# Kernel optimization log

Measured on AMD Instinct MI355X. Metric: run time of the kernel, lower is better.

The kernel has to match this reference:

```python
import jax, jax.numpy as jnp
import numpy as np
from jax import lax

B, T = 64, 2048
RNN, EMB, ATT, NF, K = 1024, 512, 128, 32, 31
PAD = (K - 1) // 2


def setup_inputs() -> dict:
    key = jax.random.key(0)
    ks = jax.random.split(key, 12)
    inp = {
        "attention_hidden_state": jax.random.normal(ks[0], (B, RNN), jnp.float32),
        "memory": jax.random.normal(ks[1], (B, T, EMB), jnp.float32),
        "processed_memory": jax.random.normal(ks[2], (B, T, ATT), jnp.float32),
        "attention_weights_cat": jax.random.uniform(ks[3], (B, 2, T), jnp.float32),
        "mask": jnp.zeros((B, T), dtype=bool),
        # query_layer: Linear(RNN -> ATT)
        "Wq": jax.random.normal(ks[4], (ATT, RNN), jnp.float32) / np.sqrt(RNN),
        "bq": jnp.zeros((ATT,), jnp.float32),
        # location conv: Conv1d(2 -> NF, kernel K, padding PAD)
        "conv_w": jax.random.normal(ks[5], (NF, 2, K), jnp.float32) / np.sqrt(2 * K),
        "conv_b": jnp.zeros((NF,), jnp.float32),
        # location dense: Linear(NF -> ATT)
        "Wl": jax.random.normal(ks[6], (ATT, NF), jnp.float32) / np.sqrt(NF),
        "bl": jnp.zeros((ATT,), jnp.float32),
        # v: Linear(ATT -> 1)
        "v_w": jax.random.normal(ks[7], (1, ATT), jnp.float32) / np.sqrt(ATT),
        "v_b": jnp.zeros((1,), jnp.float32),
    }
    return inp


def reference(attention_hidden_state, memory, processed_memory, attention_weights_cat,
              mask, Wq, bq, conv_w, conv_b, Wl, bl, v_w, v_b):
    # processed query: [B, 1, ATT]
    pq = (attention_hidden_state @ Wq.T + bq)[:, None, :]
    # location features: Conv1d over [B, 2, T] -> [B, NF, T]
    loc = lax.conv_general_dilated(
        attention_weights_cat, conv_w, window_strides=(1,),
        padding=[(PAD, PAD)], dimension_numbers=("NCH", "OIH", "NCH"))
    loc = loc + conv_b[None, :, None]
    # transpose to [B, T, NF], project to attention_dim: [B, T, ATT]
    loc = jnp.einsum("bft,af->bta", loc, Wl) + bl
    # energies: v(tanh(pq + loc + pm)) -> [B, T]
    energies = jnp.einsum("bta,a->bt", jnp.tanh(pq + loc + processed_memory), v_w[0]) + v_b[0]
    energies = jnp.where(mask, -jnp.inf, energies)
    attention_weights = jax.nn.softmax(energies, axis=1)  # [B, T]
    attention_context = jnp.einsum("bt,bte->be", attention_weights, memory)  # [B, EMB]
    return (attention_context, attention_weights)
```

## Files before the change

kernel.cpp:

```cpp
#include <hip/hip_runtime.h>
#include <math.h>

#define BB 64
#define TT 2048
#define RNN 1024
#define EMB 512
#define ATT 128
#define NF 32
#define KSZ 31
#define PAD 15

__global__ __launch_bounds__(256) void pq_kernel(
    const float* __restrict__ hidden, const float* __restrict__ Wq,
    const float* __restrict__ bq, const float* __restrict__ bl,
    float* __restrict__ pq)
{
    int b = blockIdx.x;
    __shared__ float h_s[RNN];
    int tid = threadIdx.x;
    for (int i = tid; i < RNN / 4; i += 256)
        reinterpret_cast<float4*>(h_s)[i] =
            reinterpret_cast<const float4*>(hidden + (size_t)b * RNN)[i];
    __syncthreads();
    int wave = tid >> 6, lane = tid & 63;
    int abase = blockIdx.y * 32;
    for (int a = abase + wave; a < abase + 32; a += 4) {
        const float4* wp = reinterpret_cast<const float4*>(Wq + (size_t)a * RNN);
        const float4* hp = reinterpret_cast<const float4*>(h_s);
        float acc = 0.f;
#pragma unroll
        for (int j = 0; j < 4; ++j) {
            float4 wv = wp[lane + 64 * j];
            float4 hv = hp[lane + 64 * j];
            acc += wv.x * hv.x + wv.y * hv.y + wv.z * hv.z + wv.w * hv.w;
        }
#pragma unroll
        for (int m = 32; m >= 1; m >>= 1) acc += __shfl_xor(acc, m);
        if (lane == 0) pq[b * ATT + a] = acc + bq[a] + bl[a];
    }
}

__device__ __forceinline__ float tanh_fast(float x) {
    float e2 = __expf(2.f * x);
    return 1.f - 2.f * __builtin_amdgcn_rcpf(e2 + 1.f);
}

template<int NH>
__global__ __launch_bounds__(256) void fused_kernel(
    const float* __restrict__ pm,
    const float* __restrict__ awc,
    const float* __restrict__ convw,
    const float* __restrict__ convb,
    const float* __restrict__ Wl,
    const float* __restrict__ vw,
    const float* __restrict__ vb,
    const float* __restrict__ pq,
    const float* __restrict__ memory,
    float* __restrict__ e_raw,
    float* __restrict__ part,
    float* __restrict__ ms)
{
    constexpr int TS = 64 * NH;
    const int TQv = TT / TS;
    int b  = blockIdx.x;
    int tq = blockIdx.y;
    int t0 = tq * TS;
    int tid = threadIdx.x;

    __shared__ float  awc_s[2][TS + KSZ - 1];
    __shared__ float  convw_s[NF * 2 * KSZ];
    __shared__ float  lf_s[TS][NF + 4];
    __shared__ float  e_s[64][65];
    __shared__ float  er_s[TS];
    __shared__ float  w_s[TS];
    __shared__ float  redm_s[16];
    __shared__ float4 red4_s[128];

    for (int i = tid; i < 2 * (TS + KSZ - 1); i += 256) {
        int c = i / (TS + KSZ - 1);
        int j = i - c * (TS + KSZ - 1);
        int t = t0 + j - PAD;
        awc_s[c][j] = (t >= 0 && t < TT) ? awc[((size_t)b * 2 + c) * TT + t] : 0.f;
    }
    for (int i = tid; i < NF * 2 * KSZ; i += 256)
        convw_s[i] = convw[i];
    __syncthreads();

    {
        int f = tid & 31;
        float w0[KSZ], w1[KSZ];
#pragma unroll
        for (int k = 0; k < KSZ; ++k) {
            w0[k] = convw_s[f * 2 * KSZ + k];
            w1[k] = convw_s[f * 2 * KSZ + KSZ + k];
        }
        float cb = convb[f];
#pragma unroll
        for (int half = 0; half < NH; ++half) {
            int tb = half * 64 + (tid >> 5) * 8;
            float out[8];
#pragma unroll
            for (int d = 0; d < 8; ++d) out[d] = cb;
#pragma unroll
            for (int j = 0; j < 8 + KSZ - 1; ++j) {
                float a0v = awc_s[0][tb + j];
                float a1v = awc_s[1][tb + j];
                int dlo = (j - (KSZ - 1) > 0) ? j - (KSZ - 1) : 0;
                int dhi = (j < 7) ? j : 7;
#pragma unroll
                for (int d = 0; d < 8; ++d)
                    if (d >= dlo && d <= dhi)
                        out[d] += w0[j - d] * a0v + w1[j - d] * a1v;
            }
#pragma unroll
            for (int d = 0; d < 8; ++d) lf_s[tb + d][f] = out[d];
        }
    }
    __syncthreads();

    int wave = tid >> 6, lane = tid & 63;
    int a0 = 2 * lane, a1 = a0 + 1;
    float4 wl0[NF / 4], wl1[NF / 4];
    {
        const float4* p0 = reinterpret_cast<const float4*>(Wl + (size_t)a0 * NF);
        const float4* p1 = reinterpret_cast<const float4*>(Wl + (size_t)a1 * NF);
#pragma unroll
        for (int j = 0; j < NF / 4; ++j) { wl0[j] = p0[j]; wl1[j] = p1[j]; }
    }
    float pq0 = pq[b * ATT + a0], pq1 = pq[b * ATT + a1];
    float v0  = vw[a0],           v1  = vw[a1];
    float vbv = vb[0];

#pragma unroll
    for (int half = 0; half < NH; ++half) {
        int tw = half * 64 + wave * 16;
        const float* pmb = pm + ((size_t)b * TT + t0 + tw) * ATT + a0;

        float2 pfA[8], pfB[8];
#pragma unroll
        for (int k = 0; k < 8; ++k)
            pfA[k] = *reinterpret_cast<const float2*>(pmb + (size_t)k * ATT);

#pragma unroll
        for (int i = 0; i < 8; ++i) {
            pfB[i] = *reinterpret_cast<const float2*>(pmb + (size_t)(8 + i) * ATT);
            int tl = tw + i;
            float lp0 = 0.f, lp1 = 0.f;
#pragma unroll
            for (int j = 0; j < NF / 4; ++j) {
                float4 lf = *reinterpret_cast<const float4*>(&lf_s[tl][4 * j]);
                lp0 += wl0[j].x * lf.x + wl0[j].y * lf.y + wl0[j].z * lf.z + wl0[j].w * lf.w;
                lp1 += wl1[j].x * lf.x + wl1[j].y * lf.y + wl1[j].z * lf.z + wl1[j].w * lf.w;
            }
            e_s[tl - half * 64][lane] = v0 * tanh_fast(pq0 + pfA[i].x + lp0)
                                      + v1 * tanh_fast(pq1 + pfA[i].y + lp1);
        }
#pragma unroll
        for (int i = 0; i < 8; ++i) {
            int tl = tw + 8 + i;
            float lp0 = 0.f, lp1 = 0.f;
#pragma unroll
            for (int j = 0; j < NF / 4; ++j) {
                float4 lf = *reinterpret_cast<const float4*>(&lf_s[tl][4 * j]);
                lp0 += wl0[j].x * lf.x + wl0[j].y * lf.y + wl0[j].z * lf.z + wl0[j].w * lf.w;
                lp1 += wl1[j].x * lf.x + wl1[j].y * lf.y + wl1[j].z * lf.z + wl1[j].w * lf.w;
            }
            e_s[tl - half * 64][lane] = v0 * tanh_fast(pq0 + pfB[i].x + lp0)
                                      + v1 * tanh_fast(pq1 + pfB[i].y + lp1);
        }
        __syncthreads();
        {
            int tl = tid >> 2, q = tid & 3;
            float s = 0.f;
#pragma unroll
            for (int k = 0; k < 16; ++k) s += e_s[tl][q * 16 + k];
            s += __shfl_xor(s, 1);
            s += __shfl_xor(s, 2);
            if (q == 0) {
                float raw = s + vbv;
                er_s[half * 64 + tl] = raw;
                e_raw[(size_t)b * TT + t0 + half * 64 + tl] = raw;
            }
        }
        __syncthreads();
    }

    {
        float v = (tid < TS) ? er_s[tid] : -INFINITY;
        float m = v;
#pragma unroll
        for (int d = 32; d >= 1; d >>= 1) m = fmaxf(m, __shfl_xor(m, d));
        if (NH == 2) {
            if ((tid & 63) == 0) redm_s[tid >> 6] = m;
            __syncthreads();
            m = fmaxf(redm_s[0], redm_s[1]);
        }
        float w = (tid < TS) ? __expf(v - m) : 0.f;
        if (tid < TS) w_s[tid] = w;
        float s = w;
#pragma unroll
        for (int d = 32; d >= 1; d >>= 1) s += __shfl_xor(s, d);
        if (NH == 2) {
            if ((tid & 63) == 0) redm_s[8 + (tid >> 6)] = s;
            __syncthreads();
            s = redm_s[8] + redm_s[9];
        }
        if (tid == 0) {
            ms[((size_t)b * TQv + tq) * 2 + 0] = m;
            ms[((size_t)b * TQv + tq) * 2 + 1] = s;
        }
    }
    __syncthreads();

    {
        int e4 = tid & 127, tr = tid >> 7;
        const float4* mp = reinterpret_cast<const float4*>(
            memory + ((size_t)(b * TT + t0 + tr)) * EMB) + e4;
        float4 acc = make_float4(0.f, 0.f, 0.f, 0.f);
#pragma unroll 8
        for (int i = 0; i < TS / 2; ++i) {
            float  w = w_s[2 * i + tr];
            float4 m = mp[(size_t)i * 2 * (EMB / 4)];
            acc.x += w * m.x; acc.y += w * m.y; acc.z += w * m.z; acc.w += w * m.w;
        }
        if (tr == 1) red4_s[e4] = acc;
        __syncthreads();
        if (tr == 0) {
            float4 o = red4_s[e4];
            acc.x += o.x; acc.y += o.y; acc.z += o.z; acc.w += o.w;
            reinterpret_cast<float4*>(part + ((size_t)tq * BB + b) * EMB)[e4] = acc;
        }
    }
}

template<int TQv>
__global__ __launch_bounds__(512) void finalize_kernel(
    const float* __restrict__ part, const float* __restrict__ ms,
    float* __restrict__ ctx, float* __restrict__ w_out)
{
    int b = blockIdx.x;
    int tid = threadIdx.x;
    __shared__ float scale_s[TQv];
    __shared__ float MS[2];
    if (tid < 64) {
        float m = (tid < TQv) ? ms[((size_t)b * TQv + tid) * 2 + 0] : -INFINITY;
        float s = (tid < TQv) ? ms[((size_t)b * TQv + tid) * 2 + 1] : 0.f;
        float M = m;
#pragma unroll
        for (int d = 32; d >= 1; d >>= 1) M = fmaxf(M, __shfl_xor(M, d));
        float sc = __expf(m - M);
        float Ssc = s * sc;
#pragma unroll
        for (int d = 32; d >= 1; d >>= 1) Ssc += __shfl_xor(Ssc, d);
        if (tid < TQv) scale_s[tid] = sc;
        if (tid == 0) { MS[0] = M; MS[1] = 1.f / Ssc; }
    }
    __syncthreads();
    float M = MS[0], invS = MS[1];
    {
        float acc = 0.f;
#pragma unroll
        for (int p = 0; p < TQv; ++p)
            acc += part[((size_t)p * BB + b) * EMB + tid] * scale_s[p];
        ctx[(size_t)b * EMB + tid] = acc * invS;
    }
#pragma unroll
    for (int k = 0; k < TT / 512; ++k) {
        size_t idx = (size_t)b * TT + k * 512 + tid;
        w_out[idx] = __expf(w_out[idx] - M) * invS;
    }
}

extern "C" void kernel_launch(void* const* d_in, const int* in_sizes, int n_in,
                              void* d_out, int out_size, void* d_ws, size_t ws_size,
                              hipStream_t stream)
{
    const float* hidden = (const float*)d_in[0];
    const float* memory = (const float*)d_in[1];
    const float* pm     = (const float*)d_in[2];
    const float* awc    = (const float*)d_in[3];
    const float* Wq     = (const float*)d_in[5];
    const float* bq     = (const float*)d_in[6];
    const float* convw  = (const float*)d_in[7];
    const float* convb  = (const float*)d_in[8];
    const float* Wl     = (const float*)d_in[9];
    const float* bl     = (const float*)d_in[10];
    const float* vw     = (const float*)d_in[11];
    const float* vb     = (const float*)d_in[12];

    float* out_ctx = (float*)d_out;
    float* out_w   = (float*)d_out + BB * EMB;

    float* ws = (float*)d_ws;
    float* pq = ws;

    pq_kernel<<<dim3(BB, 4), 256, 0, stream>>>(hidden, Wq, bq, bl, pq);

    size_t need32 = (size_t)(8192 + 32 * BB * EMB + BB * 32 * 2) * 4;
    if (ws_size >= need32) {
        const int TQ = 32;
        float* part  = ws + 8192;
        float* msbuf = part + (size_t)TQ * BB * EMB;
        fused_kernel<1><<<dim3(BB, TQ), 256, 0, stream>>>(
            pm, awc, convw, convb, Wl, vw, vb, pq, memory, out_w, part, msbuf);
        finalize_kernel<32><<<BB, 512, 0, stream>>>(part, msbuf, out_ctx, out_w);
    } else {
        const int TQ = 16;
        float* part  = ws + 8192;
        float* msbuf = part + (size_t)TQ * BB * EMB;
        fused_kernel<2><<<dim3(BB, TQ), 256, 0, stream>>>(
            pm, awc, convw, convb, Wl, vw, vb, pq, memory, out_w, part, msbuf);
        finalize_kernel<16><<<BB, 512, 0, stream>>>(part, msbuf, out_ctx, out_w);
    }
}
```

Before: 89.84 us.

## Warp-specialize fused attention kernel to overlap energy compute with context accumulation

Each block now covers 256 timesteps in four 64-row chunks. Waves 0-1 compute the energies for chunk h while waves 2-3 accumulate the weighted memory context for chunk h-1. An online softmax with running max and sum rescales the accumulator per chunk, and the grid shrinks to 8 time splits per batch, which cuts the partial buffers and finalize work. The cost is only half the waves doing each phase, fewer blocks (512), and serialized per-chunk barriers, which may underutilize the GPU.

```diff
diff --git a/kernel.cpp b/kernel.cpp
--- a/kernel.cpp
+++ b/kernel.cpp
@@ -9,6 +9,9 @@
 #define NF 32
 #define KSZ 31
 #define PAD 15
+#define TS 256
+#define HALVES 4
+#define TQV 8
 
 __global__ __launch_bounds__(256) void pq_kernel(
     const float* __restrict__ hidden, const float* __restrict__ Wq,
@@ -45,7 +48,6 @@
     return 1.f - 2.f * __builtin_amdgcn_rcpf(e2 + 1.f);
 }
 
-template<int NH>
 __global__ __launch_bounds__(256) void fused_kernel(
     const float* __restrict__ pm,
     const float* __restrict__ awc,
@@ -60,21 +62,18 @@
     float* __restrict__ part,
     float* __restrict__ ms)
 {
-    constexpr int TS = 64 * NH;
-    const int TQv = TT / TS;
     int b  = blockIdx.x;
     int tq = blockIdx.y;
     int t0 = tq * TS;
     int tid = threadIdx.x;
-
-    __shared__ float  awc_s[2][TS + KSZ - 1];
-    __shared__ float  convw_s[NF * 2 * KSZ];
-    __shared__ float  lf_s[TS][NF + 4];
-    __shared__ float  e_s[64][65];
-    __shared__ float  er_s[TS];
-    __shared__ float  w_s[TS];
-    __shared__ float  redm_s[16];
-    __shared__ float4 red4_s[128];
+    int wave = tid >> 6, lane = tid & 63;
+
+    __shared__ float awc_s[2][TS + KSZ - 1];
+    __shared__ float convw_s[NF * 2 * KSZ];
+    __shared__ float lf_s[TS][NF + 4];
+    __shared__ float e_s[64][68];
+    __shared__ float w_s[2][64];
+    __shared__ float sc_s[HALVES];
 
     for (int i = tid; i < 2 * (TS + KSZ - 1); i += 256) {
         int c = i / (TS + KSZ - 1);
@@ -95,8 +94,7 @@
             w1[k] = convw_s[f * 2 * KSZ + KSZ + k];
         }
         float cb = convb[f];
-#pragma unroll
-        for (int half = 0; half < NH; ++half) {
+        for (int half = 0; half < HALVES; ++half) {
             int tb = half * 64 + (tid >> 5) * 8;
             float out[8];
 #pragma unroll
@@ -116,135 +114,142 @@
             for (int d = 0; d < 8; ++d) lf_s[tb + d][f] = out[d];
         }
     }
-    __syncthreads();
-
-    int wave = tid >> 6, lane = tid & 63;
+
     int a0 = 2 * lane, a1 = a0 + 1;
     float4 wl0[NF / 4], wl1[NF / 4];
-    {
+    float pq0 = 0.f, pq1 = 0.f, v0 = 0.f, v1 = 0.f;
+    if (wave < 2) {
         const float4* p0 = reinterpret_cast<const float4*>(Wl + (size_t)a0 * NF);
         const float4* p1 = reinterpret_cast<const float4*>(Wl + (size_t)a1 * NF);
 #pragma unroll
         for (int j = 0; j < NF / 4; ++j) { wl0[j] = p0[j]; wl1[j] = p1[j]; }
-    }
-    float pq0 = pq[b * ATT + a0], pq1 = pq[b * ATT + a1];
-    float v0  = vw[a0],           v1  = vw[a1];
+        pq0 = pq[b * ATT + a0]; pq1 = pq[b * ATT + a1];
+        v0 = vw[a0]; v1 = vw[a1];
+    }
     float vbv = vb[0];
 
-#pragma unroll
-    for (int half = 0; half < NH; ++half) {
-        int tw = half * 64 + wave * 16;
-        const float* pmb = pm + ((size_t)b * TT + t0 + tw) * ATT + a0;
-
-        float2 pfA[8], pfB[8];
-#pragma unroll
-        for (int k = 0; k < 8; ++k)
-            pfA[k] = *reinterpret_cast<const float2*>(pmb + (size_t)k * ATT);
-
-#pragma unroll
-        for (int i = 0; i < 8; ++i) {
-            pfB[i] = *reinterpret_cast<const float2*>(pmb + (size_t)(8 + i) * ATT);
-            int tl = tw + i;
-            float lp0 = 0.f, lp1 = 0.f;
-#pragma unroll
-            for (int j = 0; j < NF / 4; ++j) {
-                float4 lf = *reinterpret_cast<const float4*>(&lf_s[tl][4 * j]);
-                lp0 += wl0[j].x * lf.x + wl0[j].y * lf.y + wl0[j].z * lf.z + wl0[j].w * lf.w;
-                lp1 += wl1[j].x * lf.x + wl1[j].y * lf.y + wl1[j].z * lf.z + wl1[j].w * lf.w;
-            }
-            e_s[tl - half * 64][lane] = v0 * tanh_fast(pq0 + pfA[i].x + lp0)
-                                      + v1 * tanh_fast(pq1 + pfA[i].y + lp1);
-        }
-#pragma unroll
-        for (int i = 0; i < 8; ++i) {
-            int tl = tw + 8 + i;
-            float lp0 = 0.f, lp1 = 0.f;
-#pragma unroll
-            for (int j = 0; j < NF / 4; ++j) {
-                float4 lf = *reinterpret_cast<const float4*>(&lf_s[tl][4 * j]);
-                lp0 += wl0[j].x * lf.x + wl0[j].y * lf.y + wl0[j].z * lf.z + wl0[j].w * lf.w;
-                lp1 += wl1[j].x * lf.x + wl1[j].y * lf.y + wl1[j].z * lf.z + wl1[j].w * lf.w;
-            }
-            e_s[tl - half * 64][lane] = v0 * tanh_fast(pq0 + pfB[i].x + lp0)
-                                      + v1 * tanh_fast(pq1 + pfB[i].y + lp1);
+    float m_run = -INFINITY, s_run = 0.f;
+    float4 acc = make_float4(0.f, 0.f, 0.f, 0.f);
+    int cidx = tid & 127;
+
+    __syncthreads();
+
+    for (int h = 0; h < HALVES; ++h) {
+        if (wave < 2) {
+            int rb = wave * 32;
+            const float* pmb = pm + ((size_t)b * TT + t0 + h * 64 + rb) * ATT + a0;
+            auto PROJ = [&](int r, float2 pmv) {
+                float lp0 = 0.f, lp1 = 0.f;
+#pragma unroll
+                for (int j = 0; j < NF / 4; ++j) {
+                    float4 lf = *reinterpret_cast<const float4*>(&lf_s[h * 64 + r][4 * j]);
+                    lp0 += wl0[j].x * lf.x + wl0[j].y * lf.y + wl0[j].z * lf.z + wl0[j].w * lf.w;
+                    lp1 += wl1[j].x * lf.x + wl1[j].y * lf.y + wl1[j].z * lf.z + wl1[j].w * lf.w;
+                }
+                e_s[r][lane] = v0 * tanh_fast(pq0 + pmv.x + lp0)
+                             + v1 * tanh_fast(pq1 + pmv.y + lp1);
+            };
+            float2 pfA[8], pfB[8];
+#pragma unroll
+            for (int k = 0; k < 8; ++k)
+                pfA[k] = *reinterpret_cast<const float2*>(pmb + (size_t)k * ATT);
+#pragma unroll
+            for (int i = 0; i < 8; ++i) {
+                pfB[i] = *reinterpret_cast<const float2*>(pmb + (size_t)(8 + i) * ATT);
+                PROJ(rb + i, pfA[i]);
+            }
+#pragma unroll
+            for (int i = 0; i < 8; ++i) {
+                pfA[i] = *reinterpret_cast<const float2*>(pmb + (size_t)(16 + i) * ATT);
+                PROJ(rb + 8 + i, pfB[i]);
+            }
+#pragma unroll
+            for (int i = 0; i < 8; ++i) {
+                pfB[i] = *reinterpret_cast<const float2*>(pmb + (size_t)(24 + i) * ATT);
+                PROJ(rb + 16 + i, pfA[i]);
+            }
+#pragma unroll
+            for (int i = 0; i < 8; ++i)
+                PROJ(rb + 24 + i, pfB[i]);
+        } else if (h >= 1) {
+            float sc = sc_s[h - 1];
+            acc.x *= sc; acc.y *= sc; acc.z *= sc; acc.w *= sc;
+            const float4* mp = reinterpret_cast<const float4*>(
+                memory + ((size_t)b * TT + t0 + (h - 1) * 64) * EMB) + cidx;
+#pragma unroll 8
+            for (int r = 0; r < 32; ++r) {
+                float w = w_s[(h - 1) & 1][r];
+                float4 m = mp[(size_t)r * (EMB / 4)];
+                acc.x += w * m.x; acc.y += w * m.y; acc.z += w * m.z; acc.w += w * m.w;
+            }
         }
         __syncthreads();
-        {
-            int tl = tid >> 2, q = tid & 3;
-            float s = 0.f;
-#pragma unroll
-            for (int k = 0; k < 16; ++k) s += e_s[tl][q * 16 + k];
-            s += __shfl_xor(s, 1);
-            s += __shfl_xor(s, 2);
-            if (q == 0) {
-                float raw = s + vbv;
-                er_s[half * 64 + tl] = raw;
-                e_raw[(size_t)b * TT + t0 + half * 64 + tl] = raw;
+
+        if (wave == 0) {
+            float4 s4 = make_float4(0.f, 0.f, 0.f, 0.f);
+#pragma unroll
+            for (int k = 0; k < 16; ++k) {
+                float4 x = *reinterpret_cast<const float4*>(&e_s[lane][4 * k]);
+                s4.x += x.x; s4.y += x.y; s4.z += x.z; s4.w += x.w;
+            }
+            float e = s4.x + s4.y + s4.z + s4.w + vbv;
+            e_raw[(size_t)b * TT + t0 + h * 64 + lane] = e;
+            float cm = e;
+#pragma unroll
+            for (int d = 32; d >= 1; d >>= 1) cm = fmaxf(cm, __shfl_xor(cm, d));
+            float m_new = fmaxf(m_run, cm);
+            float sc = __expf(m_run - m_new);
+            float wv = __expf(e - m_new);
+            w_s[h & 1][lane] = wv;
+            float ssum = wv;
+#pragma unroll
+            for (int d = 32; d >= 1; d >>= 1) ssum += __shfl_xor(ssum, d);
+            s_run = s_run * sc + ssum;
+            m_run = m_new;
+            if (lane == 0) sc_s[h] = sc;
+        } else if (wave >= 2 && h >= 1) {
+            const float4* mp = reinterpret_cast<const float4*>(
+                memory + ((size_t)b * TT + t0 + (h - 1) * 64) * EMB) + cidx;
+#pragma unroll 8
+            for (int r = 32; r < 64; ++r) {
+                float w = w_s[(h - 1) & 1][r];
+                float4 m = mp[(size_t)r * (EMB / 4)];
+                acc.x += w * m.x; acc.y += w * m.y; acc.z += w * m.z; acc.w += w * m.w;
             }
         }
         __syncthreads();
     }
 
-    {
-        float v = (tid < TS) ? er_s[tid] : -INFINITY;
-        float m = v;
-#pragma unroll
-        for (int d = 32; d >= 1; d >>= 1) m = fmaxf(m, __shfl_xor(m, d));
-        if (NH == 2) {
-            if ((tid & 63) == 0) redm_s[tid >> 6] = m;
-            __syncthreads();
-            m = fmaxf(redm_s[0], redm_s[1]);
-        }
-        float w = (tid < TS) ? __expf(v - m) : 0.f;
-        if (tid < TS) w_s[tid] = w;
-        float s = w;
-#pragma unroll
-        for (int d = 32; d >= 1; d >>= 1) s += __shfl_xor(s, d);
-        if (NH == 2) {
-            if ((tid & 63) == 0) redm_s[8 + (tid >> 6)] = s;
-            __syncthreads();
-            s = redm_s[8] + redm_s[9];
-        }
-        if (tid == 0) {
-            ms[((size_t)b * TQv + tq) * 2 + 0] = m;
-            ms[((size_t)b * TQv + tq) * 2 + 1] = s;
-        }
-    }
-    __syncthreads();
-
-    {
-        int e4 = tid & 127, tr = tid >> 7;
+    if (wave >= 2) {
+        float sc = sc_s[HALVES - 1];
+        acc.x *= sc; acc.y *= sc; acc.z *= sc; acc.w *= sc;
         const float4* mp = reinterpret_cast<const float4*>(
-            memory + ((size_t)(b * TT + t0 + tr)) * EMB) + e4;
-        float4 acc = make_float4(0.f, 0.f, 0.f, 0.f);
+            memory + ((size_t)b * TT + t0 + (HALVES - 1) * 64) * EMB) + cidx;
 #pragma unroll 8
-        for (int i = 0; i < TS / 2; ++i) {
-            float  w = w_s[2 * i + tr];
-            float4 m = mp[(size_t)i * 2 * (EMB / 4)];
+        for (int r = 0; r < 64; ++r) {
+            float w = w_s[(HALVES - 1) & 1][r];
+            float4 m = mp[(size_t)r * (EMB / 4)];
             acc.x += w * m.x; acc.y += w * m.y; acc.z += w * m.z; acc.w += w * m.w;
         }
-        if (tr == 1) red4_s[e4] = acc;
-        __syncthreads();
-        if (tr == 0) {
-            float4 o = red4_s[e4];
-            acc.x += o.x; acc.y += o.y; acc.z += o.z; acc.w += o.w;
-            reinterpret_cast<float4*>(part + ((size_t)tq * BB + b) * EMB)[e4] = acc;
-        }
-    }
-}
-
-template<int TQv>
+        reinterpret_cast<float4*>(part + ((size_t)tq * BB + b) * EMB)[cidx] = acc;
+    }
+    if (wave == 0 && lane == 0) {
+        ms[((size_t)b * TQV + tq) * 2 + 0] = m_run;
+        ms[((size_t)b * TQV + tq) * 2 + 1] = s_run;
+    }
+}
+
 __global__ __launch_bounds__(512) void finalize_kernel(
     const float* __restrict__ part, const float* __restrict__ ms,
     float* __restrict__ ctx, float* __restrict__ w_out)
 {
     int b = blockIdx.x;
     int tid = threadIdx.x;
-    __shared__ float scale_s[TQv];
+    __shared__ float scale_s[TQV];
     __shared__ float MS[2];
     if (tid < 64) {
-        float m = (tid < TQv) ? ms[((size_t)b * TQv + tid) * 2 + 0] : -INFINITY;
-        float s = (tid < TQv) ? ms[((size_t)b * TQv + tid) * 2 + 1] : 0.f;
+        float m = (tid < TQV) ? ms[((size_t)b * TQV + tid) * 2 + 0] : -INFINITY;
+        float s = (tid < TQV) ? ms[((size_t)b * TQV + tid) * 2 + 1] : 0.f;
         float M = m;
 #pragma unroll
         for (int d = 32; d >= 1; d >>= 1) M = fmaxf(M, __shfl_xor(M, d));
@@ -252,7 +257,7 @@
         float Ssc = s * sc;
 #pragma unroll
         for (int d = 32; d >= 1; d >>= 1) Ssc += __shfl_xor(Ssc, d);
-        if (tid < TQv) scale_s[tid] = sc;
+        if (tid < TQV) scale_s[tid] = sc;
         if (tid == 0) { MS[0] = M; MS[1] = 1.f / Ssc; }
     }
     __syncthreads();
@@ -260,7 +265,7 @@
     {
         float acc = 0.f;
 #pragma unroll
-        for (int p = 0; p < TQv; ++p)
+        for (int p = 0; p < TQV; ++p)
             acc += part[((size_t)p * BB + b) * EMB + tid] * scale_s[p];
         ctx[(size_t)b * EMB + tid] = acc * invS;
     }
@@ -291,25 +296,13 @@
     float* out_ctx = (float*)d_out;
     float* out_w   = (float*)d_out + BB * EMB;
 
-    float* ws = (float*)d_ws;
-    float* pq = ws;
+    float* ws    = (float*)d_ws;
+    float* pq    = ws;
+    float* partb = ws + 8192;
+    float* msbuf = partb + (size_t)TQV * BB * EMB;
 
     pq_kernel<<<dim3(BB, 4), 256, 0, stream>>>(hidden, Wq, bq, bl, pq);
-
-    size_t need32 = (size_t)(8192 + 32 * BB * EMB + BB * 32 * 2) * 4;
-    if (ws_size >= need32) {
-        const int TQ = 32;
-        float* part  = ws + 8192;
-        float* msbuf = part + (size_t)TQ * BB * EMB;
-        fused_kernel<1><<<dim3(BB, TQ), 256, 0, stream>>>(
-            pm, awc, convw, convb, Wl, vw, vb, pq, memory, out_w, part, msbuf);
-        finalize_kernel<32><<<BB, 512, 0, stream>>>(part, msbuf, out_ctx, out_w);
-    } else {
-        const int TQ = 16;
-        float* part  = ws + 8192;
-        float* msbuf = part + (size_t)TQ * BB * EMB;
-        fused_kernel<2><<<dim3(BB, TQ), 256, 0, stream>>>(
-            pm, awc, convw, convb, Wl, vw, vb, pq, memory, out_w, part, msbuf);
-        finalize_kernel<16><<<BB, 512, 0, stream>>>(part, msbuf, out_ctx, out_w);
-    }
-}
+    fused_kernel<<<dim3(BB, TQV), 256, 0, stream>>>(
+        pm, awc, convw, convb, Wl, vw, vb, pq, memory, out_w, partb, msbuf);
+    finalize_kernel<<<BB, 512, 0, stream>>>(partb, msbuf, out_ctx, out_w);
+}
```

New measurement: 92.22 us. 2.7% more time.

## Warp-specialize fused attention kernel into producer/consumer pipelined over time sub-tiles

Applied to the files above, without the earlier changes.

Each block now covers 512 timesteps and has 512 threads split into two roles. Producer waves compute the location conv, projection and energies for 64-step sub-tiles and prefetch the next awc window into a double buffer. Consumer waves accumulate the weighted sum over memory for the previous sub-tile in three phases between barriers. The softmax max subtraction is dropped (exp of raw energies, with the stored max set to 0), which removes a reduction but relies on the energies staying small enough not to overflow. The grid drops to 256 blocks with only four memory-streaming waves per block, which may leave too few loads in flight to saturate HBM bandwidth.

```diff
diff --git a/kernel.cpp b/kernel.cpp
--- a/kernel.cpp
+++ b/kernel.cpp
@@ -9,6 +9,9 @@
 #define NF 32
 #define KSZ 31
 #define PAD 15
+#define NS 8
+#define NGRP 4
+#define TQV 4
 
 __global__ __launch_bounds__(256) void pq_kernel(
     const float* __restrict__ hidden, const float* __restrict__ Wq,
@@ -45,8 +48,7 @@
     return 1.f - 2.f * __builtin_amdgcn_rcpf(e2 + 1.f);
 }
 
-template<int NH>
-__global__ __launch_bounds__(256) void fused_kernel(
+__global__ __launch_bounds__(512, 2) void fused_kernel(
     const float* __restrict__ pm,
     const float* __restrict__ awc,
     const float* __restrict__ convw,
@@ -60,175 +62,198 @@
     float* __restrict__ part,
     float* __restrict__ ms)
 {
-    constexpr int TS = 64 * NH;
-    const int TQv = TT / TS;
-    int b  = blockIdx.x;
-    int tq = blockIdx.y;
-    int t0 = tq * TS;
-    int tid = threadIdx.x;
-
-    __shared__ float  awc_s[2][TS + KSZ - 1];
-    __shared__ float  convw_s[NF * 2 * KSZ];
-    __shared__ float  lf_s[TS][NF + 4];
-    __shared__ float  e_s[64][65];
-    __shared__ float  er_s[TS];
-    __shared__ float  w_s[TS];
-    __shared__ float  redm_s[16];
+    int b    = blockIdx.x;
+    int grp  = blockIdx.y;
+    int tid  = threadIdx.x;
+    int wave = tid >> 6;
+    int role = wave >> 2;
+    int rtid = tid & 255;
+    int lane = rtid & 63;
+    int tg0  = grp * (NS * 64);
+
+    __shared__ float  awc_s[2][2][94];
+    __shared__ float  lf_s[64][NF + 4];
+    __shared__ float  e_s[64][68];
+    __shared__ float  w_s[2][64];
     __shared__ float4 red4_s[128];
 
-    for (int i = tid; i < 2 * (TS + KSZ - 1); i += 256) {
-        int c = i / (TS + KSZ - 1);
-        int j = i - c * (TS + KSZ - 1);
-        int t = t0 + j - PAD;
-        awc_s[c][j] = (t >= 0 && t < TT) ? awc[((size_t)b * 2 + c) * TT + t] : 0.f;
-    }
-    for (int i = tid; i < NF * 2 * KSZ; i += 256)
-        convw_s[i] = convw[i];
+    if (tid < 188) {
+        int c = (tid >= 94) ? 1 : 0;
+        int j = tid - 94 * c;
+        int t = tg0 + j - PAD;
+        awc_s[0][c][j] = (t >= 0 && t < TT) ? awc[((size_t)b * 2 + c) * TT + t] : 0.f;
+    }
+    float  cw0[KSZ], cw1[KSZ], cb = 0.f;
+    float4 wl0[NF / 4], wl1[NF / 4];
+    float  pq0 = 0.f, pq1 = 0.f, v0 = 0.f, v1 = 0.f;
+    int a0 = 2 * lane;
+    if (role == 0) {
+        int f = rtid & 31;
+#pragma unroll
+        for (int k = 0; k < KSZ; ++k) {
+            cw0[k] = convw[f * 2 * KSZ + k];
+            cw1[k] = convw[f * 2 * KSZ + KSZ + k];
+        }
+        cb = convb[f];
+        const float4* p0 = reinterpret_cast<const float4*>(Wl + (size_t)a0 * NF);
+        const float4* p1 = reinterpret_cast<const float4*>(Wl + (size_t)(a0 + 1) * NF);
+#pragma unroll
+        for (int j = 0; j < NF / 4; ++j) { wl0[j] = p0[j]; wl1[j] = p1[j]; }
+        pq0 = pq[b * ATT + a0]; pq1 = pq[b * ATT + a0 + 1];
+        v0  = vw[a0];           v1  = vw[a0 + 1];
+    }
+    float vbv = vb[0];
+    float4 acc = make_float4(0.f, 0.f, 0.f, 0.f);
+    float  s_tot = 0.f;
+    int ccol = rtid & 127, parity = rtid >> 7;
+    const float* membase = memory + ((size_t)b * TT + tg0) * EMB;
     __syncthreads();
 
-    {
-        int f = tid & 31;
-        float w0[KSZ], w1[KSZ];
-#pragma unroll
-        for (int k = 0; k < KSZ; ++k) {
-            w0[k] = convw_s[f * 2 * KSZ + k];
-            w1[k] = convw_s[f * 2 * KSZ + KSZ + k];
-        }
-        float cb = convb[f];
-#pragma unroll
-        for (int half = 0; half < NH; ++half) {
-            int tb = half * 64 + (tid >> 5) * 8;
-            float out[8];
-#pragma unroll
-            for (int d = 0; d < 8; ++d) out[d] = cb;
-#pragma unroll
-            for (int j = 0; j < 8 + KSZ - 1; ++j) {
-                float a0v = awc_s[0][tb + j];
-                float a1v = awc_s[1][tb + j];
-                int dlo = (j - (KSZ - 1) > 0) ? j - (KSZ - 1) : 0;
-                int dhi = (j < 7) ? j : 7;
-#pragma unroll
-                for (int d = 0; d < 8; ++d)
-                    if (d >= dlo && d <= dhi)
-                        out[d] += w0[j - d] * a0v + w1[j - d] * a1v;
-            }
-#pragma unroll
-            for (int d = 0; d < 8; ++d) lf_s[tb + d][f] = out[d];
-        }
-    }
+    for (int k = 0; k <= NS; ++k) {
+        int km1 = (k >= 1) ? k - 1 : 0;
+        const float* mrow = membase + (size_t)km1 * 64 * EMB;
+        int wbc = km1 & 1;
+
+        if (role == 0) {
+            if (k < NS) {
+                int f = rtid & 31, tb = (rtid >> 5) * 8;
+                const float (*ab)[94] = awc_s[k & 1];
+                float out[8];
+#pragma unroll
+                for (int d = 0; d < 8; ++d) out[d] = cb;
+#pragma unroll
+                for (int j = 0; j < 8 + KSZ - 1; ++j) {
+                    float x0 = ab[0][tb + j], x1 = ab[1][tb + j];
+                    int dlo = (j - (KSZ - 1) > 0) ? j - (KSZ - 1) : 0;
+                    int dhi = (j < 7) ? j : 7;
+#pragma unroll
+                    for (int d = 0; d < 8; ++d)
+                        if (d >= dlo && d <= dhi)
+                            out[d] += cw0[j - d] * x0 + cw1[j - d] * x1;
+                }
+#pragma unroll
+                for (int d = 0; d < 8; ++d) lf_s[tb + d][f] = out[d];
+            }
+        } else if (k >= 1) {
+            if (rtid < 64) {
+                float wv = w_s[wbc][lane];
+#pragma unroll
+                for (int d = 32; d >= 1; d >>= 1) wv += __shfl_xor(wv, d);
+                s_tot += wv;
+            }
+#pragma unroll
+            for (int p = 0; p < 11; ++p) {
+                int r = 2 * p + parity;
+                float wv = w_s[wbc][r];
+                float4 m = *reinterpret_cast<const float4*>(
+                    mrow + (size_t)r * EMB + 4 * ccol);
+                acc.x += wv * m.x; acc.y += wv * m.y;
+                acc.z += wv * m.z; acc.w += wv * m.w;
+            }
+        }
+        __syncthreads();
+
+        if (role == 0) {
+            float av = 0.f; int c2 = 0, j2 = 0;
+            bool doA = (k + 1 < NS) && (rtid < 188);
+            if (doA) {
+                c2 = (rtid >= 94) ? 1 : 0; j2 = rtid - 94 * c2;
+                int t = tg0 + (k + 1) * 64 + j2 - PAD;
+                av = (t >= 0 && t < TT) ? awc[((size_t)b * 2 + c2) * TT + t] : 0.f;
+            }
+            if (k < NS) {
+                int pw = rtid >> 6;
+                const float* pmb = pm + ((size_t)b * TT + tg0 + k * 64 + pw * 16) * ATT + a0;
+                float2 pfA[8], pfB[8];
+#pragma unroll
+                for (int q = 0; q < 8; ++q)
+                    pfA[q] = *reinterpret_cast<const float2*>(pmb + (size_t)q * ATT);
+#pragma unroll
+                for (int i = 0; i < 8; ++i) {
+                    pfB[i] = *reinterpret_cast<const float2*>(pmb + (size_t)(8 + i) * ATT);
+                    int tl = pw * 16 + i;
+                    float lp0 = 0.f, lp1 = 0.f;
+#pragma unroll
+                    for (int j = 0; j < NF / 4; ++j) {
+                        float4 lf = *reinterpret_cast<const float4*>(&lf_s[tl][4 * j]);
+                        lp0 += wl0[j].x * lf.x + wl0[j].y * lf.y + wl0[j].z * lf.z + wl0[j].w * lf.w;
+                        lp1 += wl1[j].x * lf.x + wl1[j].y * lf.y + wl1[j].z * lf.z + wl1[j].w * lf.w;
+                    }
+                    e_s[tl][lane] = v0 * tanh_fast(pq0 + pfA[i].x + lp0)
+                                  + v1 * tanh_fast(pq1 + pfA[i].y + lp1);
+                }
+#pragma unroll
+                for (int i = 0; i < 8; ++i) {
+                    int tl = pw * 16 + 8 + i;
+                    float lp0 = 0.f, lp1 = 0.f;
+#pragma unroll
+                    for (int j = 0; j < NF / 4; ++j) {
+                        float4 lf = *reinterpret_cast<const float4*>(&lf_s[tl][4 * j]);
+                        lp0 += wl0[j].x * lf.x + wl0[j].y * lf.y + wl0[j].z * lf.z + wl0[j].w * lf.w;
+                        lp1 += wl1[j].x * lf.x + wl1[j].y * lf.y + wl1[j].z * lf.z + wl1[j].w * lf.w;
+                    }
+                    e_s[tl][lane] = v0 * tanh_fast(pq0 + pfB[i].x + lp0)
+                                  + v1 * tanh_fast(pq1 + pfB[i].y + lp1);
+                }
+            }
+            if (doA) awc_s[(k + 1) & 1][c2][j2] = av;
+        } else if (k >= 1) {
+#pragma unroll
+            for (int p = 11; p < 22; ++p) {
+                int r = 2 * p + parity;
+                float wv = w_s[wbc][r];
+                float4 m = *reinterpret_cast<const float4*>(
+                    mrow + (size_t)r * EMB + 4 * ccol);
+                acc.x += wv * m.x; acc.y += wv * m.y;
+                acc.z += wv * m.z; acc.w += wv * m.w;
+            }
+        }
+        __syncthreads();
+
+        if (role == 0) {
+            if (k < NS) {
+                int t = rtid >> 2, q = rtid & 3;
+                const float* er = &e_s[t][q * 16];
+                float4 x0 = *reinterpret_cast<const float4*>(er);
+                float4 x1 = *reinterpret_cast<const float4*>(er + 4);
+                float4 x2 = *reinterpret_cast<const float4*>(er + 8);
+                float4 x3 = *reinterpret_cast<const float4*>(er + 12);
+                float s = x0.x + x0.y + x0.z + x0.w + x1.x + x1.y + x1.z + x1.w
+                        + x2.x + x2.y + x2.z + x2.w + x3.x + x3.y + x3.z + x3.w;
+                s += __shfl_xor(s, 1);
+                s += __shfl_xor(s, 2);
+                if (q == 0) {
+                    float raw = s + vbv;
+                    e_raw[(size_t)b * TT + tg0 + k * 64 + t] = raw;
+                    w_s[k & 1][t] = __expf(raw);
+                }
+            }
+        } else if (k >= 1) {
+#pragma unroll
+            for (int p = 22; p < 32; ++p) {
+                int r = 2 * p + parity;
+                float wv = w_s[wbc][r];
+                float4 m = *reinterpret_cast<const float4*>(
+                    mrow + (size_t)r * EMB + 4 * ccol);
+                acc.x += wv * m.x; acc.y += wv * m.y;
+                acc.z += wv * m.z; acc.w += wv * m.w;
+            }
+        }
+        __syncthreads();
+    }
+
+    if (role == 1 && parity == 1) red4_s[ccol] = acc;
     __syncthreads();
-
-    int wave = tid >> 6, lane = tid & 63;
-    int a0 = 2 * lane, a1 = a0 + 1;
-    float4 wl0[NF / 4], wl1[NF / 4];
-    {
-        const float4* p0 = reinterpret_cast<const float4*>(Wl + (size_t)a0 * NF);
-        const float4* p1 = reinterpret_cast<const float4*>(Wl + (size_t)a1 * NF);
-#pragma unroll
-        for (int j = 0; j < NF / 4; ++j) { wl0[j] = p0[j]; wl1[j] = p1[j]; }
-    }
-    float pq0 = pq[b * ATT + a0], pq1 = pq[b * ATT + a1];
-    float v0  = vw[a0],           v1  = vw[a1];
-    float vbv = vb[0];
-
-#pragma unroll
-    for (int half = 0; half < NH; ++half) {
-        int tw = half * 64 + wave * 16;
-        const float* pmb = pm + ((size_t)b * TT + t0 + tw) * ATT + a0;
-
-        float2 pfA[8], pfB[8];
-#pragma unroll
-        for (int k = 0; k < 8; ++k)
-            pfA[k] = *reinterpret_cast<const float2*>(pmb + (size_t)k * ATT);
-
-#pragma unroll
-        for (int i = 0; i < 8; ++i) {
-            pfB[i] = *reinterpret_cast<const float2*>(pmb + (size_t)(8 + i) * ATT);
-            int tl = tw + i;
-            float lp0 = 0.f, lp1 = 0.f;
-#pragma unroll
-            for (int j = 0; j < NF / 4; ++j) {
-                float4 lf = *reinterpret_cast<const float4*>(&lf_s[tl][4 * j]);
-                lp0 += wl0[j].x * lf.x + wl0[j].y * lf.y + wl0[j].z * lf.z + wl0[j].w * lf.w;
-                lp1 += wl1[j].x * lf.x + wl1[j].y * lf.y + wl1[j].z * lf.z + wl1[j].w * lf.w;
-            }
-            e_s[tl - half * 64][lane] = v0 * tanh_fast(pq0 + pfA[i].x + lp0)
-                                      + v1 * tanh_fast(pq1 + pfA[i].y + lp1);
-        }
-#pragma unroll
-        for (int i = 0; i < 8; ++i) {
-            int tl = tw + 8 + i;
-            float lp0 = 0.f, lp1 = 0.f;
-#pragma unroll
-            for (int j = 0; j < NF / 4; ++j) {
-                float4 lf = *reinterpret_cast<const float4*>(&lf_s[tl][4 * j]);
-                lp0 += wl0[j].x * lf.x + wl0[j].y * lf.y + wl0[j].z * lf.z + wl0[j].w * lf.w;
-                lp1 += wl1[j].x * lf.x + wl1[j].y * lf.y + wl1[j].z * lf.z + wl1[j].w * lf.w;
-            }
-            e_s[tl - half * 64][lane] = v0 * tanh_fast(pq0 + pfB[i].x + lp0)
-                                      + v1 * tanh_fast(pq1 + pfB[i].y + lp1);
-        }
-        __syncthreads();
-        {
-            int tl = tid >> 2, q = tid & 3;
-            float s = 0.f;
-#pragma unroll
-            for (int k = 0; k < 16; ++k) s += e_s[tl][q * 16 + k];
-            s += __shfl_xor(s, 1);
-            s += __shfl_xor(s, 2);
-            if (q == 0) {
-                float raw = s + vbv;
-                er_s[half * 64 + tl] = raw;
-                e_raw[(size_t)b * TT + t0 + half * 64 + tl] = raw;
-            }
-        }
-        __syncthreads();
-    }
-
-    {
-        float v = (tid < TS) ? er_s[tid] : -INFINITY;
-        float m = v;
-#pragma unroll
-        for (int d = 32; d >= 1; d >>= 1) m = fmaxf(m, __shfl_xor(m, d));
-        if (NH == 2) {
-            if ((tid & 63) == 0) redm_s[tid >> 6] = m;
-            __syncthreads();
-            m = fmaxf(redm_s[0], redm_s[1]);
-        }
-        float w = (tid < TS) ? __expf(v - m) : 0.f;
-        if (tid < TS) w_s[tid] = w;
-        float s = w;
-#pragma unroll
-        for (int d = 32; d >= 1; d >>= 1) s += __shfl_xor(s, d);
-        if (NH == 2) {
-            if ((tid & 63) == 0) redm_s[8 + (tid >> 6)] = s;
-            __syncthreads();
-            s = redm_s[8] + redm_s[9];
-        }
-        if (tid == 0) {
-            ms[((size_t)b * TQv + tq) * 2 + 0] = m;
-            ms[((size_t)b * TQv + tq) * 2 + 1] = s;
-        }
-    }
-    __syncthreads();
-
-    {
-        int e4 = tid & 127, tr = tid >> 7;
-        const float4* mp = reinterpret_cast<const float4*>(
-            memory + ((size_t)(b * TT + t0 + tr)) * EMB) + e4;
-        float4 acc = make_float4(0.f, 0.f, 0.f, 0.f);
-#pragma unroll 8
-        for (int i = 0; i < TS / 2; ++i) {
-            float  w = w_s[2 * i + tr];
-            float4 m = mp[(size_t)i * 2 * (EMB / 4)];
-            acc.x += w * m.x; acc.y += w * m.y; acc.z += w * m.z; acc.w += w * m.w;
-        }
-        if (tr == 1) red4_s[e4] = acc;
-        __syncthreads();
-        if (tr == 0) {
-            float4 o = red4_s[e4];
+    if (role == 1) {
+        if (parity == 0) {
+            float4 o = red4_s[ccol];
             acc.x += o.x; acc.y += o.y; acc.z += o.z; acc.w += o.w;
-            reinterpret_cast<float4*>(part + ((size_t)tq * BB + b) * EMB)[e4] = acc;
+            *reinterpret_cast<float4*>(
+                part + ((size_t)grp * BB + b) * EMB + 4 * ccol) = acc;
+        }
+        if (rtid == 0) {
+            ms[((size_t)b * TQV + grp) * 2 + 0] = 0.f;
+            ms[((size_t)b * TQV + grp) * 2 + 1] = s_tot;
         }
     }
 }
@@ -291,25 +316,13 @@
     float* out_ctx = (float*)d_out;
     float* out_w   = (float*)d_out + BB * EMB;
 
-    float* ws = (float*)d_ws;
-    float* pq = ws;
+    float* ws    = (float*)d_ws;
+    float* pq    = ws;
+    float* partb = ws + 8192;
+    float* msbuf = partb + (size_t)NGRP * BB * EMB;
 
     pq_kernel<<<dim3(BB, 4), 256, 0, stream>>>(hidden, Wq, bq, bl, pq);
-
-    size_t need32 = (size_t)(8192 + 32 * BB * EMB + BB * 32 * 2) * 4;
-    if (ws_size >= need32) {
-        const int TQ = 32;
-        float* part  = ws + 8192;
-        float* msbuf = part + (size_t)TQ * BB * EMB;
-        fused_kernel<1><<<dim3(BB, TQ), 256, 0, stream>>>(
-            pm, awc, convw, convb, Wl, vw, vb, pq, memory, out_w, part, msbuf);
-        finalize_kernel<32><<<BB, 512, 0, stream>>>(part, msbuf, out_ctx, out_w);
-    } else {
-        const int TQ = 16;
-        float* part  = ws + 8192;
-        float* msbuf = part + (size_t)TQ * BB * EMB;
-        fused_kernel<2><<<dim3(BB, TQ), 256, 0, stream>>>(
-            pm, awc, convw, convb, Wl, vw, vb, pq, memory, out_w, part, msbuf);
-        finalize_kernel<16><<<BB, 512, 0, stream>>>(part, msbuf, out_ctx, out_w);
-    }
-}
+    fused_kernel<<<dim3(BB, NGRP), 512, 0, stream>>>(
+        pm, awc, convw, convb, Wl, vw, vb, pq, memory, out_w, partb, msbuf);
+    finalize_kernel<TQV><<<BB, 512, 0, stream>>>(partb, msbuf, out_ctx, out_w);
+}
```

After: 125.9 us. 40.1% more time.
